# Performance work log

Measured on AMD Instinct MI355X. Metric: run time of the kernel, lower is better.

The kernel has to match this reference:

```python
import jax, jax.numpy as jnp
import numpy as np

DEPTH = 3
MAX_NB = 10
HIDDEN = 128


def setup_inputs() -> dict:
    key = jax.random.key(0)
    k = jax.random.split(key, 14)
    B, A, E, H, NB = 64, 1024, 2048, HIDDEN, MAX_NB
    s = 0.05
    return {
        "input_atom": jax.random.normal(k[0], (B, A, 82), jnp.float32),
        "input_bond": jax.random.normal(k[1], (B, E, 6), jnp.float32),
        "atom_graph": jax.random.randint(k[2], (B, A, NB), 0, A),
        "bond_graph": jax.random.randint(k[3], (B, A, NB), 0, E),
        "num_nbs": jax.random.randint(k[4], (B, A), 0, NB + 1),
        "node_mask": jnp.ones((B, A), jnp.float32),
        "W_atom": jax.random.normal(k[5], (82, H), jnp.float32) * s,
        "W_nei_atom": jax.random.normal(k[6], (H, H), jnp.float32) * s,
        "W_nei_bond": jax.random.normal(k[7], (6, H), jnp.float32) * s,
        "W_self": jax.random.normal(k[8], (H, H), jnp.float32) * s,
        "W_U2": jax.random.normal(k[9], (H + 6, H), jnp.float32) * s,
        "b_U2": jax.random.normal(k[10], (H,), jnp.float32) * s,
        "W_U1": jax.random.normal(k[11], (2 * H, H), jnp.float32) * s,
        "b_U1": jax.random.normal(k[12], (H,), jnp.float32) * s,
    }


def reference(input_atom, input_bond, atom_graph, bond_graph, num_nbs, node_mask,
              W_atom, W_nei_atom, W_nei_bond, W_self, W_U2, b_U2, W_U1, b_U1):
    B, A, NB = atom_graph.shape
    H = W_atom.shape[1]
    atom_features = input_atom @ W_atom                       # [B, A, H]
    # neighbor validity mask: [B, A, NB, 1]
    mask_nei = (jnp.arange(NB)[None, None, :] < num_nbs[:, :, None]).astype(jnp.float32)[..., None]
    idx_a = atom_graph.reshape(B, A * NB, 1)
    idx_b = bond_graph.reshape(B, A * NB, 1)
    # bond neighbor features are loop-invariant: gather once
    fbond_nei = jnp.take_along_axis(input_bond, idx_b, axis=1).reshape(B, A, NB, 6)
    h_nei_bond = fbond_nei @ W_nei_bond                       # [B, A, NB, H]
    node_m = node_mask[..., None]                             # [B, A, 1]
    kernel = None
    for _ in range(DEPTH):
        fatom_nei = jnp.take_along_axis(atom_features, idx_a, axis=1).reshape(B, A, NB, H)
        h_nei = (fatom_nei @ W_nei_atom) * h_nei_bond         # [B, A, NB, H]
        f_nei = jnp.sum(h_nei * mask_nei, axis=2)             # [B, A, H]
        f_self = atom_features @ W_self                        # [B, A, H]
        kernel = f_nei * f_self * node_m
        l_nei = jnp.concatenate([fatom_nei, fbond_nei], axis=3)  # [B, A, NB, H+6]
        pre_label = l_nei @ W_U2 + b_U2
        nei_label = jnp.sum(pre_label * mask_nei, axis=2)      # [B, A, H]
        new_label = jnp.concatenate([atom_features, nei_label], axis=2)
        atom_features = new_label @ W_U1 + b_U1
    return kernel, atom_features
```

## Files before the change

kernel.cpp:

```cpp
#include <hip/hip_runtime.h>

constexpr int NB = 10, H = 128;
constexpr int M = 64 * 1024;
constexpr long SL = (long)M * H;

typedef __attribute__((ext_vector_type(8))) short s16x8;
typedef __attribute__((ext_vector_type(4))) float f32x4;

__device__ __forceinline__ ushort f2b(float f) {
    union { float f; uint u; } v; v.f = f;
    uint u = v.u;
    uint r = u + 0x7fffu + ((u >> 16) & 1u);
    return (ushort)(r >> 16);
}
__device__ __forceinline__ float b2f(ushort u) {
    union { uint u; float f; } v; v.u = ((uint)u) << 16; return v.f;
}

__device__ __forceinline__ int swz(int bid, int cpx) {
    return (bid & 7) * cpx + (bid >> 3);
}

template<int NC, int FLAGS>
__device__ __forceinline__ void gemm_body(
    int tg, const ushort* __restrict__ Abf, const ushort* __restrict__ WT,
    const ushort* __restrict__ FNb, const float* __restrict__ nmask,
    float* __restrict__ Cf, ushort* __restrict__ Cb)
{
    constexpr bool KOUT = FLAGS & 8, OF32 = FLAGS & 16;
    constexpr int K = NC * 32;
    const int lane = threadIdx.x & 63, wid = threadIdx.x >> 6;
    const int l15 = lane & 15, g = lane >> 4;

    s16x8 w[2][NC];
    #pragma unroll
    for (int ct = 0; ct < 2; ++ct)
        #pragma unroll
        for (int kc = 0; kc < NC; ++kc)
            w[ct][kc] = *(const s16x8*)(WT + (size_t)((2 * wid + ct) * 16 + l15) * K + kc * 32 + g * 8);

    #pragma unroll
    for (int i = 0; i < 4; ++i) {
        const int m0 = (tg * 4 + i) * 16;
        s16x8 ac[NC];
        #pragma unroll
        for (int kc = 0; kc < NC; ++kc)
            ac[kc] = *(const s16x8*)(Abf + (size_t)(m0 + l15) * K + kc * 32 + g * 8);

        f32x4 acc[2];
        #pragma unroll
        for (int ct = 0; ct < 2; ++ct) acc[ct] = (f32x4){0.f, 0.f, 0.f, 0.f};
        #pragma unroll
        for (int kc = 0; kc < NC; ++kc)
            #pragma unroll
            for (int ct = 0; ct < 2; ++ct)
                acc[ct] = __builtin_amdgcn_mfma_f32_16x16x32_bf16(ac[kc], w[ct][kc], acc[ct], 0, 0, 0);

        #pragma unroll
        for (int ct = 0; ct < 2; ++ct) {
            const int col = (2 * wid + ct) * 16 + l15;
            #pragma unroll
            for (int r = 0; r < 4; ++r) {
                const int m = m0 + 4 * g + r;
                const size_t o = (size_t)m * H + col;
                float v = acc[ct][r];
                if constexpr (KOUT) v = v * b2f(FNb[o]) * nmask[m];
                if constexpr (OF32) Cf[o] = v; else Cb[o] = f2b(v);
            }
        }
    }
}

template<bool OF32>
__device__ __forceinline__ void u1f_body(
    int tg, const ushort* __restrict__ AF, const ushort* __restrict__ SATOM,
    const ushort* __restrict__ FBSb, const ushort* __restrict__ WT,
    float* __restrict__ Cf, ushort* __restrict__ Cb)
{
    const int lane = threadIdx.x & 63, wid = threadIdx.x >> 6;
    const int l15 = lane & 15, g = lane >> 4;

    s16x8 w[2][9];
    #pragma unroll
    for (int ct = 0; ct < 2; ++ct)
        #pragma unroll
        for (int kc = 0; kc < 9; ++kc)
            w[ct][kc] = *(const s16x8*)(WT + (size_t)((2 * wid + ct) * 16 + l15) * 288 + kc * 32 + g * 8);

    #pragma unroll
    for (int i = 0; i < 4; ++i) {
        const int m0 = (tg * 4 + i) * 16;
        const size_t rb = (size_t)(m0 + l15) * H + g * 8;
        s16x8 ac[9];
        #pragma unroll
        for (int kc = 0; kc < 4; ++kc) {
            ac[kc]     = *(const s16x8*)(AF    + rb + kc * 32);
            ac[kc + 4] = *(const s16x8*)(SATOM + rb + kc * 32);
        }
        ac[8] = (s16x8){0,0,0,0,0,0,0,0};
        if (g == 0) ac[8] = *(const s16x8*)(FBSb + (size_t)(m0 + l15) * 8);

        f32x4 acc[2];
        #pragma unroll
        for (int ct = 0; ct < 2; ++ct) acc[ct] = (f32x4){0.f, 0.f, 0.f, 0.f};
        #pragma unroll
        for (int kc = 0; kc < 9; ++kc)
            #pragma unroll
            for (int ct = 0; ct < 2; ++ct)
                acc[ct] = __builtin_amdgcn_mfma_f32_16x16x32_bf16(ac[kc], w[ct][kc], acc[ct], 0, 0, 0);

        #pragma unroll
        for (int ct = 0; ct < 2; ++ct) {
            const int col = (2 * wid + ct) * 16 + l15;
            #pragma unroll
            for (int r = 0; r < 4; ++r) {
                const size_t o = (size_t)(m0 + 4 * g + r) * H + col;
                if constexpr (OF32) Cf[o] = acc[ct][r]; else Cb[o] = f2b(acc[ct][r]);
            }
        }
    }
}

template<int NC, int FLAGS>
__global__ __launch_bounds__(256, 4) void gemm_af(
    const ushort* __restrict__ Abf, const ushort* __restrict__ WT,
    const ushort* __restrict__ FNb, const float* __restrict__ nmask,
    float* __restrict__ Cf, ushort* __restrict__ Cb)
{
    gemm_body<NC, FLAGS>(swz(blockIdx.x, 128), Abf, WT, FNb, nmask, Cf, Cb);
}

template<bool OF32>
__global__ __launch_bounds__(256, 4) void u1f(
    const ushort* __restrict__ AF, const ushort* __restrict__ SATOM,
    const ushort* __restrict__ FBSb, const ushort* __restrict__ WT,
    float* __restrict__ Cf, ushort* __restrict__ Cb)
{
    u1f_body<OF32>(swz(blockIdx.x, 128), AF, SATOM, FBSb, WT, Cf, Cb);
}

__global__ __launch_bounds__(256, 4) void final2(
    const ushort* __restrict__ AF, const ushort* __restrict__ SATl,
    const ushort* __restrict__ FBSb, const ushort* __restrict__ WTu1f,
    const ushort* __restrict__ WTslf, const ushort* __restrict__ FNEIb,
    const float* __restrict__ nmask, float* __restrict__ out1,
    float* __restrict__ out0)
{
    if (blockIdx.x < 1024)
        u1f_body<true>(swz(blockIdx.x, 128), AF, SATl, FBSb, WTu1f, out1, nullptr);
    else
        gemm_body<4, 8 | 16>(swz(blockIdx.x - 1024, 128), AF, WTslf, FNEIb,
                             nmask, out0, nullptr);
}

__global__ __launch_bounds__(256, 8) void gather_satom(
    const ushort* __restrict__ AF, const int* __restrict__ ag,
    const int* __restrict__ nn, ushort* __restrict__ SATOM)
{
    const int bid = swz(blockIdx.x, 512);
    const int m  = bid * 16 + (threadIdx.x >> 4);
    const int c8 = (threadIdx.x & 15) * 8;
    const int b  = m >> 10;
    const int nnb = nn[m];
    const ushort* AFb = AF + ((size_t)b << 10) * H + c8;
    const int* agm = ag + (size_t)m * NB;

    int2 iv0 = *(const int2*)(agm + 0);
    int2 iv1 = *(const int2*)(agm + 2);
    int2 iv2 = *(const int2*)(agm + 4);
    int2 iv3 = *(const int2*)(agm + 6);
    int2 iv4 = *(const int2*)(agm + 8);

    float sacc[8];
    #pragma unroll
    for (int i = 0; i < 8; ++i) sacc[i] = 0.f;

    #define GS_STEP(nb, ia)                                              \
    if ((nb) < nnb) {                                                    \
        s16x8 av = *(const s16x8*)(AFb + (size_t)(ia) * H);              \
        _Pragma("unroll")                                                \
        for (int i = 0; i < 8; ++i) sacc[i] += b2f((ushort)av[i]);       \
    }
    GS_STEP(0, iv0.x) GS_STEP(1, iv0.y)
    GS_STEP(2, iv1.x) GS_STEP(3, iv1.y)
    GS_STEP(4, iv2.x) GS_STEP(5, iv2.y)
    GS_STEP(6, iv3.x) GS_STEP(7, iv3.y)
    GS_STEP(8, iv4.x) GS_STEP(9, iv4.y)
    #undef GS_STEP

    s16x8 so;
    #pragma unroll
    for (int i = 0; i < 8; ++i) so[i] = (short)f2b(sacc[i]);
    *(s16x8*)(SATOM + (size_t)m * H + c8) = so;
}

__global__ __launch_bounds__(256, 4) void gather_last(
    const ushort* __restrict__ AF, const ushort* __restrict__ ATW,
    const ushort* __restrict__ HB, const int* __restrict__ ag,
    const int* __restrict__ bg, const int* __restrict__ nn,
    ushort* __restrict__ SATOM, ushort* __restrict__ FNEIb)
{
    const int bid = swz(blockIdx.x, 512);
    const int m  = bid * 16 + (threadIdx.x >> 4);
    const int c8 = (threadIdx.x & 15) * 8;
    const int b  = m >> 10;
    const int nnb = nn[m];
    const ushort* AFb  = AF  + ((size_t)b << 10) * H + c8;
    const ushort* ATWb = ATW + ((size_t)b << 10) * H + c8;
    const ushort* HBb  = HB  + ((size_t)b << 11) * H + c8;
    const int* agm = ag + (size_t)m * NB;
    const int* bgm = bg + (size_t)m * NB;

    int2 ia0 = *(const int2*)(agm + 0), ib0 = *(const int2*)(bgm + 0);
    int2 ia1 = *(const int2*)(agm + 2), ib1 = *(const int2*)(bgm + 2);
    int2 ia2 = *(const int2*)(agm + 4), ib2 = *(const int2*)(bgm + 4);
    int2 ia3 = *(const int2*)(agm + 6), ib3 = *(const int2*)(bgm + 6);
    int2 ia4 = *(const int2*)(agm + 8), ib4 = *(const int2*)(bgm + 8);

    float sacc[8], facc[8];
    #pragma unroll
    for (int i = 0; i < 8; ++i) { sacc[i] = 0.f; facc[i] = 0.f; }

    #define GL_STEP(nb, ia, ib)                                          \
    if ((nb) < nnb) {                                                    \
        s16x8 av = *(const s16x8*)(AFb  + (size_t)(ia) * H);             \
        s16x8 tv = *(const s16x8*)(ATWb + (size_t)(ia) * H);             \
        s16x8 hv = *(const s16x8*)(HBb  + (size_t)(ib) * H);             \
        _Pragma("unroll")                                                \
        for (int i = 0; i < 8; ++i) {                                    \
            sacc[i] += b2f((ushort)av[i]);                               \
            facc[i] += b2f((ushort)tv[i]) * b2f((ushort)hv[i]);          \
        }                                                                \
    }
    GL_STEP(0, ia0.x, ib0.x) GL_STEP(1, ia0.y, ib0.y)
    GL_STEP(2, ia1.x, ib1.x) GL_STEP(3, ia1.y, ib1.y)
    GL_STEP(4, ia2.x, ib2.x) GL_STEP(5, ia2.y, ib2.y)
    GL_STEP(6, ia3.x, ib3.x) GL_STEP(7, ia3.y, ib3.y)
    GL_STEP(8, ia4.x, ib4.x) GL_STEP(9, ia4.y, ib4.y)
    #undef GL_STEP

    s16x8 so, fo;
    #pragma unroll
    for (int i = 0; i < 8; ++i) { so[i] = (short)f2b(sacc[i]); fo[i] = (short)f2b(facc[i]); }
    *(s16x8*)(SATOM + (size_t)m * H + c8) = so;
    *(s16x8*)(FNEIb + (size_t)m * H + c8) = fo;
}

__device__ __forceinline__ void fa_body(
    int tg, const float* __restrict__ ia, const float* __restrict__ Wa,
    ushort* __restrict__ Cb)
{
    const int lane = threadIdx.x & 63, wid = threadIdx.x >> 6;
    const int l15 = lane & 15, g = lane >> 4;

    s16x8 w[2][3];
    #pragma unroll
    for (int ct = 0; ct < 2; ++ct) {
        const int n = (2 * wid + ct) * 16 + l15;
        #pragma unroll
        for (int kc = 0; kc < 3; ++kc) {
            s16x8 wv;
            #pragma unroll
            for (int i = 0; i < 8; ++i) {
                const int k = kc * 32 + g * 8 + i;
                wv[i] = (short)(k < 82 ? f2b(Wa[k * H + n]) : 0);
            }
            w[ct][kc] = wv;
        }
    }

    #pragma unroll
    for (int t = 0; t < 4; ++t) {
        const int m0 = (tg * 4 + t) * 16;
        const float* row = ia + (size_t)(m0 + l15) * 82;
        s16x8 a[3];
        #pragma unroll
        for (int kc = 0; kc < 3; ++kc) {
            #pragma unroll
            for (int p = 0; p < 4; ++p) {
                const int k = kc * 32 + g * 8 + 2 * p;
                float2 v = (k < 82) ? *(const float2*)(row + k)
                                    : make_float2(0.f, 0.f);
                a[kc][2 * p]     = (short)f2b(v.x);
                a[kc][2 * p + 1] = (short)f2b(v.y);
            }
        }
        f32x4 acc[2];
        #pragma unroll
        for (int ct = 0; ct < 2; ++ct) acc[ct] = (f32x4){0.f, 0.f, 0.f, 0.f};
        #pragma unroll
        for (int kc = 0; kc < 3; ++kc)
            #pragma unroll
            for (int ct = 0; ct < 2; ++ct)
                acc[ct] = __builtin_amdgcn_mfma_f32_16x16x32_bf16(a[kc], w[ct][kc], acc[ct], 0, 0, 0);
        #pragma unroll
        for (int ct = 0; ct < 2; ++ct) {
            const int col = (2 * wid + ct) * 16 + l15;
            #pragma unroll
            for (int r = 0; r < 4; ++r)
                Cb[(size_t)(m0 + 4 * g + r) * H + col] = f2b(acc[ct][r]);
        }
    }
}

__global__ __launch_bounds__(256, 4) void k0_prep_fa(
    const float* __restrict__ ia, const float* __restrict__ Wa,
    const float* __restrict__ Wna, const float* __restrict__ Ws,
    const float* __restrict__ Wu2, const float* __restrict__ bu2,
    const float* __restrict__ Wu1, const float* __restrict__ bu1,
    const float* __restrict__ bond, const int* __restrict__ bg,
    const int* __restrict__ nn, const float* __restrict__ Wnb,
    ushort* __restrict__ AF0, ushort* __restrict__ WTs,
    ushort* __restrict__ FBSb, ushort* __restrict__ HB)
{
    const int bid = blockIdx.x;
    if (bid < 1024) {
        fa_body(swz(bid, 128), ia, Wa, AF0);
    } else if (bid < 1296) {
        int t = (bid - 1024) * 256 + threadIdx.x;
        const int tid = t;
        if (t < 128 * 128) { int n = t / 128, k = t % 128;
            WTs[tid] = f2b(Wna[k * H + n]); return; }
        t -= 128 * 128;
        if (t < 128 * 128) { int n = t / 128, k = t % 128;
            WTs[tid] = f2b(Ws[k * H + n]); return; }
        t -= 128 * 128;
        {
            const int n = t / 288, k = t % 288;
            float v = 0.f;
            if (k < 128) {
                v = Wu1[k * H + n];
            } else if (k < 256) {
                const int kk = k - 128;
                float s = 0.f;
                for (int j = 0; j < 128; ++j) s += Wu2[kk * H + j] * Wu1[(128 + j) * H + n];
                v = s;
            } else {
                const int j = k - 256;
                if (j < 6) {
                    float s = 0.f;
                    for (int q = 0; q < 128; ++q) s += Wu2[(128 + j) * H + q] * Wu1[(128 + q) * H + n];
                    v = s;
                } else if (j == 6) {
                    float s = 0.f;
                    for (int q = 0; q < 128; ++q) s += bu2[q] * Wu1[(128 + q) * H + n];
                    v = s;
                } else if (j == 7) {
                    v = bu1[n];
                }
            }
            WTs[tid] = f2b(v);
            return;
        }
    } else if (bid < 1552) {
        const int m = (bid - 1296) * 256 + threadIdx.x;
        const int b = m >> 10;
        const int nnb = nn[m];
        float s[6] = {0,0,0,0,0,0};
        for (int nb = 0; nb < nnb; ++nb) {
            const int ib = bg[m * NB + nb];
            const float* fb = bond + ((size_t)(b << 11) + (size_t)ib) * 6;
            #pragma unroll
            for (int j = 0; j < 6; ++j) s[j] += fb[j];
        }
        s16x8 o;
        #pragma unroll
        for (int j = 0; j < 6; ++j) o[j] = (short)f2b(s[j]);
        o[6] = (short)f2b((float)nnb);
        o[7] = (short)f2b(1.0f);
        *(s16x8*)(FBSb + (size_t)m * 8) = o;
    } else {
        const int t = (bid - 1552) * 256 + threadIdx.x;
        const int r = t >> 4, c8 = (t & 15) * 8;
        const float* fb = bond + (size_t)r * 6;
        const float2 f01 = *(const float2*)fb;
        const float2 f23 = *(const float2*)(fb + 2);
        const float2 f45 = *(const float2*)(fb + 4);
        s16x8 o;
        #pragma unroll
        for (int i = 0; i < 8; ++i) {
            const int c = c8 + i;
            const float v = f01.x * Wnb[0 * H + c] + f01.y * Wnb[1 * H + c]
                          + f23.x * Wnb[2 * H + c] + f23.y * Wnb[3 * H + c]
                          + f45.x * Wnb[4 * H + c] + f45.y * Wnb[5 * H + c];
            o[i] = (short)f2b(v);
        }
        *(s16x8*)(HB + (size_t)r * H + c8) = o;
    }
}

extern "C" void kernel_launch(void* const* d_in, const int* in_sizes, int n_in,
                              void* d_out, int out_size, void* d_ws, size_t ws_size,
                              hipStream_t stream)
{
    (void)in_sizes; (void)n_in; (void)out_size; (void)ws_size;

    const float* input_atom = (const float*)d_in[0];
    const float* input_bond = (const float*)d_in[1];
    const int*   atom_graph = (const int*)d_in[2];
    const int*   bond_graph = (const int*)d_in[3];
    const int*   num_nbs    = (const int*)d_in[4];
    const float* node_mask  = (const float*)d_in[5];
    const float* W_atom     = (const float*)d_in[6];
    const float* W_nei_atom = (const float*)d_in[7];
    const float* W_nei_bond = (const float*)d_in[8];
    const float* W_self     = (const float*)d_in[9];
    const float* W_U2       = (const float*)d_in[10];
    const float* b_U2       = (const float*)d_in[11];
    const float* W_U1       = (const float*)d_in[12];
    const float* b_U1       = (const float*)d_in[13];

    char* ws = (char*)d_ws;
    const size_t MB = 1024 * 1024;
    ushort* AF0   = (ushort*)(ws);
    ushort* AF1   = (ushort*)(ws + 16 * MB);
    ushort* SATw  = (ushort*)(ws + 32 * MB);
    ushort* ATW   = SATw;
    ushort* HB    = (ushort*)(ws + 64 * MB);
    ushort* SATl  = (ushort*)(ws + 96 * MB);
    ushort* FBSb  = (ushort*)(ws + 112 * MB);
    ushort* WTs_  = (ushort*)(ws + 113 * MB);

    ushort* WTna  = WTs_;
    ushort* WTslf = WTna  + 128 * 128;
    ushort* WTu1f = WTslf + 128 * 128;

    float*  out0  = (float*)d_out;
    float*  out1  = out0 + SL;
    ushort* FNEIb = AF1;

    k0_prep_fa<<<9744, 256, 0, stream>>>(input_atom, W_atom, W_nei_atom,
                                         W_self, W_U2, b_U2, W_U1, b_U1,
                                         input_bond, bond_graph, num_nbs,
                                         W_nei_bond, AF0, WTs_, FBSb, HB);

    gather_satom<<<4096, 256, 0, stream>>>(AF0, atom_graph, num_nbs, SATw);
    u1f<false><<<1024, 256, 0, stream>>>(AF0, SATw, FBSb, WTu1f, nullptr, AF1);
    gather_satom<<<4096, 256, 0, stream>>>(AF1, atom_graph, num_nbs, SATw);
    u1f<false><<<1024, 256, 0, stream>>>(AF1, SATw, FBSb, WTu1f, nullptr, AF0);

    gemm_af<4, 0><<<1024, 256, 0, stream>>>(AF0, WTna, nullptr, nullptr,
                                            nullptr, ATW);
    gather_last<<<4096, 256, 0, stream>>>(AF0, ATW, HB, atom_graph, bond_graph,
                                          num_nbs, SATl, FNEIb);
    final2<<<2048, 256, 0, stream>>>(AF0, SATl, FBSb, WTu1f, WTslf, FNEIb,
                                     node_mask, out1, out0);
}
```

Baseline: 186.7 us.

## Transpose MFMA outputs for vector stores and split last gather across kernels

Swaps the MFMA operand order so each lane holds four consecutive output columns of one row, so epilogues write 4-wide vector stores (and load FNb as a vector) instead of scattered scalar stores. The last-layer atom-sum gather is moved into the same launch as the W_nei_atom GEMM (block-range split), and the remaining gather only computes the bond-weighted neighbor sum. This cuts store transactions and shortens the heavier gather, at the cost of reading AF twice across kernels and a larger mixed launch.

```diff
diff --git a/kernel.cpp b/kernel.cpp
--- a/kernel.cpp
+++ b/kernel.cpp
@@ -5,6 +5,7 @@
 constexpr long SL = (long)M * H;
 
 typedef __attribute__((ext_vector_type(8))) short s16x8;
+typedef __attribute__((ext_vector_type(4))) short s16x4;
 typedef __attribute__((ext_vector_type(4))) float f32x4;
 
 __device__ __forceinline__ ushort f2b(float f) {
@@ -54,18 +55,28 @@
         for (int kc = 0; kc < NC; ++kc)
             #pragma unroll
             for (int ct = 0; ct < 2; ++ct)
-                acc[ct] = __builtin_amdgcn_mfma_f32_16x16x32_bf16(ac[kc], w[ct][kc], acc[ct], 0, 0, 0);
-
+                acc[ct] = __builtin_amdgcn_mfma_f32_16x16x32_bf16(w[ct][kc], ac[kc], acc[ct], 0, 0, 0);
+
+        const int m = m0 + l15;
+        float nm;
+        if constexpr (KOUT) nm = nmask[m];
         #pragma unroll
         for (int ct = 0; ct < 2; ++ct) {
-            const int col = (2 * wid + ct) * 16 + l15;
-            #pragma unroll
-            for (int r = 0; r < 4; ++r) {
-                const int m = m0 + 4 * g + r;
-                const size_t o = (size_t)m * H + col;
-                float v = acc[ct][r];
-                if constexpr (KOUT) v = v * b2f(FNb[o]) * nmask[m];
-                if constexpr (OF32) Cf[o] = v; else Cb[o] = f2b(v);
+            const int col = (2 * wid + ct) * 16 + 4 * g;
+            const size_t o = (size_t)m * H + col;
+            f32x4 v = acc[ct];
+            if constexpr (KOUT) {
+                s16x4 fv = *(const s16x4*)(FNb + o);
+                #pragma unroll
+                for (int r = 0; r < 4; ++r) v[r] = v[r] * b2f((ushort)fv[r]) * nm;
+            }
+            if constexpr (OF32) {
+                *(f32x4*)(Cf + o) = v;
+            } else {
+                s16x4 ov;
+                #pragma unroll
+                for (int r = 0; r < 4; ++r) ov[r] = (short)f2b(v[r]);
+                *(s16x4*)(Cb + o) = ov;
             }
         }
     }
@@ -107,15 +118,20 @@
         for (int kc = 0; kc < 9; ++kc)
             #pragma unroll
             for (int ct = 0; ct < 2; ++ct)
-                acc[ct] = __builtin_amdgcn_mfma_f32_16x16x32_bf16(ac[kc], w[ct][kc], acc[ct], 0, 0, 0);
-
+                acc[ct] = __builtin_amdgcn_mfma_f32_16x16x32_bf16(w[ct][kc], ac[kc], acc[ct], 0, 0, 0);
+
+        const int m = m0 + l15;
         #pragma unroll
         for (int ct = 0; ct < 2; ++ct) {
-            const int col = (2 * wid + ct) * 16 + l15;
-            #pragma unroll
-            for (int r = 0; r < 4; ++r) {
-                const size_t o = (size_t)(m0 + 4 * g + r) * H + col;
-                if constexpr (OF32) Cf[o] = acc[ct][r]; else Cb[o] = f2b(acc[ct][r]);
+            const int col = (2 * wid + ct) * 16 + 4 * g;
+            const size_t o = (size_t)m * H + col;
+            if constexpr (OF32) {
+                *(f32x4*)(Cf + o) = acc[ct];
+            } else {
+                s16x4 ov;
+                #pragma unroll
+                for (int r = 0; r < 4; ++r) ov[r] = (short)f2b(acc[ct][r]);
+                *(s16x4*)(Cb + o) = ov;
             }
         }
     }
@@ -153,11 +169,10 @@
                              nmask, out0, nullptr);
 }
 
-__global__ __launch_bounds__(256, 8) void gather_satom(
-    const ushort* __restrict__ AF, const int* __restrict__ ag,
+__device__ __forceinline__ void satom_body(
+    int bid, const ushort* __restrict__ AF, const int* __restrict__ ag,
     const int* __restrict__ nn, ushort* __restrict__ SATOM)
 {
-    const int bid = swz(blockIdx.x, 512);
     const int m  = bid * 16 + (threadIdx.x >> 4);
     const int c8 = (threadIdx.x & 15) * 8;
     const int b  = m >> 10;
@@ -194,18 +209,35 @@
     *(s16x8*)(SATOM + (size_t)m * H + c8) = so;
 }
 
-__global__ __launch_bounds__(256, 4) void gather_last(
-    const ushort* __restrict__ AF, const ushort* __restrict__ ATW,
-    const ushort* __restrict__ HB, const int* __restrict__ ag,
-    const int* __restrict__ bg, const int* __restrict__ nn,
-    ushort* __restrict__ SATOM, ushort* __restrict__ FNEIb)
+__global__ __launch_bounds__(256, 8) void gather_satom(
+    const ushort* __restrict__ AF, const int* __restrict__ ag,
+    const int* __restrict__ nn, ushort* __restrict__ SATOM)
+{
+    satom_body(swz(blockIdx.x, 512), AF, ag, nn, SATOM);
+}
+
+__global__ __launch_bounds__(256, 4) void k5_atw_sat(
+    const ushort* __restrict__ AF, const ushort* __restrict__ WTna,
+    const int* __restrict__ ag, const int* __restrict__ nn,
+    ushort* __restrict__ ATW, ushort* __restrict__ SATl)
+{
+    if (blockIdx.x < 1024)
+        gemm_body<4, 0>(swz(blockIdx.x, 128), AF, WTna, nullptr, nullptr,
+                        nullptr, ATW);
+    else
+        satom_body(swz(blockIdx.x - 1024, 512), AF, ag, nn, SATl);
+}
+
+__global__ __launch_bounds__(256, 8) void gather_fnei(
+    const ushort* __restrict__ ATW, const ushort* __restrict__ HB,
+    const int* __restrict__ ag, const int* __restrict__ bg,
+    const int* __restrict__ nn, ushort* __restrict__ FNEIb)
 {
     const int bid = swz(blockIdx.x, 512);
     const int m  = bid * 16 + (threadIdx.x >> 4);
     const int c8 = (threadIdx.x & 15) * 8;
     const int b  = m >> 10;
     const int nnb = nn[m];
-    const ushort* AFb  = AF  + ((size_t)b << 10) * H + c8;
     const ushort* ATWb = ATW + ((size_t)b << 10) * H + c8;
     const ushort* HBb  = HB  + ((size_t)b << 11) * H + c8;
     const int* agm = ag + (size_t)m * NB;
@@ -217,32 +249,28 @@
     int2 ia3 = *(const int2*)(agm + 6), ib3 = *(const int2*)(bgm + 6);
     int2 ia4 = *(const int2*)(agm + 8), ib4 = *(const int2*)(bgm + 8);
 
-    float sacc[8], facc[8];
-    #pragma unroll
-    for (int i = 0; i < 8; ++i) { sacc[i] = 0.f; facc[i] = 0.f; }
-
-    #define GL_STEP(nb, ia, ib)                                          \
-    if ((nb) < nnb) {                                                    \
-        s16x8 av = *(const s16x8*)(AFb  + (size_t)(ia) * H);             \
-        s16x8 tv = *(const s16x8*)(ATWb + (size_t)(ia) * H);             \
-        s16x8 hv = *(const s16x8*)(HBb  + (size_t)(ib) * H);             \
-        _Pragma("unroll")                                                \
-        for (int i = 0; i < 8; ++i) {                                    \
-            sacc[i] += b2f((ushort)av[i]);                               \
-            facc[i] += b2f((ushort)tv[i]) * b2f((ushort)hv[i]);          \
-        }                                                                \
-    }
-    GL_STEP(0, ia0.x, ib0.x) GL_STEP(1, ia0.y, ib0.y)
-    GL_STEP(2, ia1.x, ib1.x) GL_STEP(3, ia1.y, ib1.y)
-    GL_STEP(4, ia2.x, ib2.x) GL_STEP(5, ia2.y, ib2.y)
-    GL_STEP(6, ia3.x, ib3.x) GL_STEP(7, ia3.y, ib3.y)
-    GL_STEP(8, ia4.x, ib4.x) GL_STEP(9, ia4.y, ib4.y)
-    #undef GL_STEP
-
-    s16x8 so, fo;
-    #pragma unroll
-    for (int i = 0; i < 8; ++i) { so[i] = (short)f2b(sacc[i]); fo[i] = (short)f2b(facc[i]); }
-    *(s16x8*)(SATOM + (size_t)m * H + c8) = so;
+    float facc[8];
+    #pragma unroll
+    for (int i = 0; i < 8; ++i) facc[i] = 0.f;
+
+    #define GF_STEP(nb, ia, ib)                                           \
+    if ((nb) < nnb) {                                                     \
+        s16x8 tv = *(const s16x8*)(ATWb + (size_t)(ia) * H);              \
+        s16x8 hv = *(const s16x8*)(HBb  + (size_t)(ib) * H);              \
+        _Pragma("unroll")                                                 \
+        for (int i = 0; i < 8; ++i)                                       \
+            facc[i] += b2f((ushort)tv[i]) * b2f((ushort)hv[i]);           \
+    }
+    GF_STEP(0, ia0.x, ib0.x) GF_STEP(1, ia0.y, ib0.y)
+    GF_STEP(2, ia1.x, ib1.x) GF_STEP(3, ia1.y, ib1.y)
+    GF_STEP(4, ia2.x, ib2.x) GF_STEP(5, ia2.y, ib2.y)
+    GF_STEP(6, ia3.x, ib3.x) GF_STEP(7, ia3.y, ib3.y)
+    GF_STEP(8, ia4.x, ib4.x) GF_STEP(9, ia4.y, ib4.y)
+    #undef GF_STEP
+
+    s16x8 fo;
+    #pragma unroll
+    for (int i = 0; i < 8; ++i) fo[i] = (short)f2b(facc[i]);
     *(s16x8*)(FNEIb + (size_t)m * H + c8) = fo;
 }
 
@@ -292,13 +320,15 @@
         for (int kc = 0; kc < 3; ++kc)
             #pragma unroll
             for (int ct = 0; ct < 2; ++ct)
-                acc[ct] = __builtin_amdgcn_mfma_f32_16x16x32_bf16(a[kc], w[ct][kc], acc[ct], 0, 0, 0);
+                acc[ct] = __builtin_amdgcn_mfma_f32_16x16x32_bf16(w[ct][kc], a[kc], acc[ct], 0, 0, 0);
+        const int m = m0 + l15;
         #pragma unroll
         for (int ct = 0; ct < 2; ++ct) {
-            const int col = (2 * wid + ct) * 16 + l15;
-            #pragma unroll
-            for (int r = 0; r < 4; ++r)
-                Cb[(size_t)(m0 + 4 * g + r) * H + col] = f2b(acc[ct][r]);
+            const int col = (2 * wid + ct) * 16 + 4 * g;
+            s16x4 ov;
+            #pragma unroll
+            for (int r = 0; r < 4; ++r) ov[r] = (short)f2b(acc[ct][r]);
+            *(s16x4*)(Cb + (size_t)m * H + col) = ov;
         }
     }
 }
@@ -439,10 +469,10 @@
     gather_satom<<<4096, 256, 0, stream>>>(AF1, atom_graph, num_nbs, SATw);
     u1f<false><<<1024, 256, 0, stream>>>(AF1, SATw, FBSb, WTu1f, nullptr, AF0);
 
-    gemm_af<4, 0><<<1024, 256, 0, stream>>>(AF0, WTna, nullptr, nullptr,
-                                            nullptr, ATW);
-    gather_last<<<4096, 256, 0, stream>>>(AF0, ATW, HB, atom_graph, bond_graph,
-                                          num_nbs, SATl, FNEIb);
+    k5_atw_sat<<<5120, 256, 0, stream>>>(AF0, WTna, atom_graph, num_nbs,
+                                         ATW, SATl);
+    gather_fnei<<<4096, 256, 0, stream>>>(ATW, HB, atom_graph, bond_graph,
+                                          num_nbs, FNEIb);
     final2<<<2048, 256, 0, stream>>>(AF0, SATl, FBSb, WTu1f, WTslf, FNEIb,
                                      node_mask, out1, out0);
 }
```

Result: slower. 200.3 us (+7.3%).
